# Kernel optimization log

Hardware: AMD Instinct MI355X
Metric: run time of the kernel (lower is better)

Reference implementation:

```python
import jax, jax.numpy as jnp
import numpy as np

DIM = 768
HID = 1536
EPS = 1e-12
SCALE = float(np.sqrt(DIM))


def _layernorm(x, gamma, beta):
    mu = jnp.mean(x, axis=-1, keepdims=True)
    var = jnp.mean(jnp.square(x - mu), axis=-1, keepdims=True)
    return (x - mu) * jax.lax.rsqrt(var + EPS) * gamma + beta


def setup_inputs() -> dict:
    key = jax.random.key(0)
    ks = jax.random.split(key, 16)
    s = 1.0 / np.sqrt(DIM)
    sh = 1.0 / np.sqrt(HID)
    x = jax.random.normal(ks[0], (8, 2048, DIM), dtype=jnp.float32)
    return {
        "x": x,
        "Wq": jax.random.uniform(ks[1], (DIM, DIM), jnp.float32, -s, s),
        "bq": jax.random.uniform(ks[2], (DIM,), jnp.float32, -s, s),
        "Wk": jax.random.uniform(ks[3], (DIM, DIM), jnp.float32, -s, s),
        "bk": jax.random.uniform(ks[4], (DIM,), jnp.float32, -s, s),
        "Wv": jax.random.uniform(ks[5], (DIM, DIM), jnp.float32, -s, s),
        "bv": jax.random.uniform(ks[6], (DIM,), jnp.float32, -s, s),
        "Wp": jax.random.uniform(ks[7], (DIM, DIM), jnp.float32, -s, s),
        "bp": jax.random.uniform(ks[8], (DIM,), jnp.float32, -s, s),
        "g1": jnp.ones((DIM,), jnp.float32),
        "be1": jnp.zeros((DIM,), jnp.float32),
        "W1": jax.random.uniform(ks[9], (HID, DIM), jnp.float32, -s, s),
        "b1": jax.random.uniform(ks[10], (HID,), jnp.float32, -s, s),
        "W2": jax.random.uniform(ks[11], (DIM, HID), jnp.float32, -sh, sh),
        "b2": jax.random.uniform(ks[12], (DIM,), jnp.float32, -sh, sh),
        "g2": jnp.ones((DIM,), jnp.float32),
        "be2": jnp.zeros((DIM,), jnp.float32),
    }


def reference(x, Wq, bq, Wk, bk, Wv, bv, Wp, bp, g1, be1, W1, b1, W2, b2, g2, be2):
    # NOTE: original code does NOT split into heads; single full-dim bmm attention.
    Q = jnp.einsum("bsd,ed->bse", x, Wq) + bq  # [B,S,D]
    K = jnp.einsum("bsd,ed->bse", x, Wk) + bk
    V = jnp.einsum("bsd,ed->bse", x, Wv) + bv
    alpha = jnp.einsum("bqd,bkd->bqk", Q, K) / SCALE  # [B,S,S]
    alpha = jax.nn.softmax(alpha, axis=-1)
    attn = jnp.einsum("bqk,bkd->bqd", alpha, V)
    attn = jnp.einsum("bsd,ed->bse", attn, Wp) + bp  # linear_proj
    h = _layernorm(x + attn, g1, be1)
    mlp = jax.nn.gelu(jnp.einsum("bsd,hd->bsh", h, W1) + b1, approximate=False)
    mlp = jnp.einsum("bsh,dh->bsd", mlp, W2) + b2
    return _layernorm(h + mlp, g2, be2)
```

## Files before the change

kernel.cpp:

```cpp
#include <hip/hip_runtime.h>
#include <math.h>

#define D_MODEL 768
#define D_HID   1536
#define N_BATCH 8
#define SEQLEN  2048
#define NROWS   (N_BATCH*SEQLEN)

typedef unsigned short u16;
typedef unsigned char  u8;
typedef __attribute__((ext_vector_type(8))) short bfrag;
typedef __attribute__((ext_vector_type(4))) float facc;

__device__ __forceinline__ u16 f2bf(float f) {
  unsigned u = __float_as_uint(f);
  u += 0x7fffu + ((u >> 16) & 1u);
  return (u16)(u >> 16);
}
__device__ __forceinline__ float bf2f(u16 u) {
  return __uint_as_float((unsigned)u << 16);
}
__device__ __forceinline__ u8 f2fp8(float f) {
  return (u8)(__builtin_amdgcn_cvt_pk_fp8_f32(f, f, 0, 0) & 0xff);
}

__device__ __forceinline__ void async16(const void* g, void* l) {
  __builtin_amdgcn_global_load_lds((const __attribute__((address_space(1))) void*)g,
                                   (__attribute__((address_space(3))) void*)l,
                                   16, 0, 0);
}
__device__ __forceinline__ void wg_barrier() {
  asm volatile("" ::: "memory");
  __builtin_amdgcn_s_barrier();
  asm volatile("" ::: "memory");
}
#define VMCNT(n) asm volatile("s_waitcnt vmcnt(" #n ")" ::: "memory")

__global__ __launch_bounds__(256) void cvt_all(
    const float* __restrict__ x,  const float* __restrict__ Wq,
    const float* __restrict__ Wk, const float* __restrict__ Wv,
    const float* __restrict__ Wp, const float* __restrict__ W1,
    const float* __restrict__ W2, const float* __restrict__ bq,
    const float* __restrict__ bk, const float* __restrict__ bv,
    u16* __restrict__ XB, u16* __restrict__ WQKV, u16* __restrict__ WPB,
    u16* __restrict__ W1B, u16* __restrict__ W2B, float* __restrict__ BQKV,
    float* __restrict__ LSUM) {
  long i = (long)blockIdx.x * 256 + threadIdx.x;
  const float* src; u16* dst; long off;
  if      (i < 3145728) { src = x;  dst = XB;             off = i; }
  else if (i < 3293184) { src = Wq; dst = WQKV;           off = i - 3145728; }
  else if (i < 3440640) { src = Wk; dst = WQKV + 589824;  off = i - 3293184; }
  else if (i < 3588096) { src = Wv; dst = WQKV + 1179648; off = i - 3440640; }
  else if (i < 3735552) { src = Wp; dst = WPB;            off = i - 3588096; }
  else if (i < 4030464) { src = W1; dst = W1B;            off = i - 3735552; }
  else if (i < 4325376) { src = W2; dst = W2B;            off = i - 4030464; }
  else if (i < 4325952) {
    long j = i - 4325376;
    const float* s = (j < 192) ? bq : (j < 384) ? bk : bv;
    long o = (j < 192) ? j : (j < 384) ? j - 192 : j - 384;
    ((float4*)BQKV)[j] = ((const float4*)s)[o];
    return;
  } else if (i < 4330048) {
    float4 zz = {0.f, 0.f, 0.f, 0.f};
    ((float4*)LSUM)[i - 4325952] = zz;
    return;
  } else return;
  float4 v = ((const float4*)src)[off];
  ushort4 o4;
  o4.x = f2bf(v.x); o4.y = f2bf(v.y); o4.z = f2bf(v.z); o4.w = f2bf(v.w);
  *reinterpret_cast<ushort4*>(dst + off * 4) = o4;
}

enum { EPI_EXP = 1, EPI_DIV = 2, EPI_GELU = 4, EPI_QKV = 5, EPI_RES = 6 };

template<int EPI>
__global__ __launch_bounds__(512, 2)
void gemm8(const u16* __restrict__ Aall, const u16* __restrict__ Ball,
           void* __restrict__ Cout,
           int M, int N, int K,
           long sA, long sB, long sC,
           const float* __restrict__ bias,
           const u16* __restrict__ resid,
           float* __restrict__ lsum,
           float scale)
{
  __shared__ __align__(16) char smem[131072];
  const int z = blockIdx.z;
  const u16* A = Aall + (long)z * sA;
  const u16* B = Ball + (long)z * sB;
  const int bm = blockIdx.x, bn = blockIdx.y;
  const int tid = (int)threadIdx.x;
  const int lane = tid & 63, wv = tid >> 6;
  const int wr = wv >> 2, wc = wv & 3;

  facc acc[8][4] = {};

  const int srow = tid >> 3;
  const int scol = (((tid & 7) ^ (srow & 7)) << 3);
  const u16* Abase = A + (long)(bm * 256) * K;
  const u16* Bbase = B + (long)(bn * 256) * K;
  const int fr = lane & 15, g0 = lane >> 4;
  const int nt = K >> 6;

  auto STAGE = [&](int t, int b) {
    u16* Asb = (u16*)(smem + b * 65536);
    u16* Bsb = (u16*)(smem + b * 65536 + 32768);
    const long k0 = (long)t * 64;
#pragma unroll
    for (int p = 0; p < 4; ++p)
      async16(Abase + (long)(p * 64 + srow) * K + k0 + scol, Asb + p * 4096 + wv * 512);
#pragma unroll
    for (int p = 0; p < 4; ++p)
      async16(Bbase + (long)(p * 64 + srow) * K + k0 + scol, Bsb + p * 4096 + wv * 512);
  };

#define G8_LDA(mh)                                                              \
  _Pragma("unroll") for (int i = 0; i < 4; ++i)                                 \
  _Pragma("unroll") for (int h = 0; h < 2; ++h) {                               \
    const int r = wr * 128 + (mh) * 64 + i * 16 + fr;                           \
    af[i][h] = *(const bfrag*)(As + r * 64 + (((g0 + h * 4) ^ (r & 7)) << 3));  \
  }
#define G8_LDB(nh)                                                              \
  _Pragma("unroll") for (int j = 0; j < 2; ++j)                                 \
  _Pragma("unroll") for (int h = 0; h < 2; ++h) {                               \
    const int r = wc * 64 + (nh) * 32 + j * 16 + fr;                            \
    bfv[j][h] = *(const bfrag*)(Bs + r * 64 + (((g0 + h * 4) ^ (r & 7)) << 3)); \
  }
#define G8_FMA(mh, nh)                                                          \
  __builtin_amdgcn_s_setprio(1);                                                \
  _Pragma("unroll") for (int i = 0; i < 4; ++i)                                 \
  _Pragma("unroll") for (int j = 0; j < 2; ++j)                                 \
  _Pragma("unroll") for (int h = 0; h < 2; ++h)                                 \
    acc[(mh) * 4 + i][(nh) * 2 + j] = __builtin_amdgcn_mfma_f32_16x16x32_bf16(  \
        af[i][h], bfv[j][h], acc[(mh) * 4 + i][(nh) * 2 + j], 0, 0, 0);         \
  __builtin_amdgcn_s_setprio(0);

  STAGE(0, 0);
  for (int t = 0; t < nt; ++t) {
    const int ct = t & 1;
    const u16* As = (const u16*)(smem + ct * 65536);
    const u16* Bs = (const u16*)(smem + ct * 65536 + 32768);
    if (t + 1 < nt) { STAGE(t + 1, ct ^ 1); VMCNT(8); }
    else            { VMCNT(0); }
    wg_barrier();
    bfrag af[4][2], bfv[2][2];
    G8_LDA(0) G8_LDB(0) G8_FMA(0, 0) wg_barrier();
    G8_LDB(1)           G8_FMA(0, 1) wg_barrier();
    G8_LDA(1)           G8_FMA(1, 1) wg_barrier();
    G8_LDB(0)           G8_FMA(1, 0) wg_barrier();
  }
#undef G8_LDA
#undef G8_LDB
#undef G8_FMA

  const int rb = bm * 256 + wr * 128;
  const int cb = bn * 256 + wc * 64;
  const int quad = lane >> 4;

  if constexpr (EPI == EPI_QKV) {
    const int c64 = bn * 4 + wc;
    const int which = c64 / 12;
    float bj[4];
#pragma unroll
    for (int j = 0; j < 4; ++j) bj[j] = bias[cb + j * 16 + fr];
    if (which == 2) {
      u8* VT_ = (u8*)resid;
      const int zb = rb >> 11;
      const int sbase = rb & 2047;
      const int dimb = (c64 - 24) * 64;
#pragma unroll
      for (int i = 0; i < 8; ++i)
#pragma unroll
        for (int j = 0; j < 4; ++j) {
          const int dim = dimb + j * 16 + fr;
          unsigned v01 = __builtin_amdgcn_cvt_pk_fp8_f32(acc[i][j][0] + bj[j],
                                                         acc[i][j][1] + bj[j], 0, 0);
          unsigned v23 = __builtin_amdgcn_cvt_pk_fp8_f32(acc[i][j][2] + bj[j],
                                                         acc[i][j][3] + bj[j], 0, 0);
          unsigned w = (v01 & 0xffffu) | (v23 << 16);
          *reinterpret_cast<unsigned*>(VT_ + (long)zb * D_MODEL * SEQLEN +
                                       (long)dim * SEQLEN + sbase + i * 16 + quad * 4) = w;
        }
      return;
    }
    u8* ep8 = (u8*)(smem + wv * 8192);
    u8* Cg = (u8*)Cout + (long)which * NROWS * D_MODEL;
    const int cbo = (c64 - which * 12) * 64;
#pragma unroll
    for (int i = 0; i < 8; ++i)
#pragma unroll
      for (int r = 0; r < 4; ++r) {
        const int lrow = i * 16 + quad * 4 + r;
#pragma unroll
        for (int j = 0; j < 4; ++j)
          ep8[lrow * 64 + j * 16 + fr] = f2fp8(acc[i][j][r] + bj[j]);
      }
#pragma unroll
    for (int it = 0; it < 8; ++it) {
      const int lr = it * 16 + (lane >> 2);
      const int ch = (lane & 3) << 4;
      int4 d = *(const int4*)(ep8 + lr * 64 + ch);
      *reinterpret_cast<int4*>(Cg + (long)(rb + lr) * D_MODEL + cbo + ch) = d;
    }
  } else if constexpr (EPI == EPI_GELU) {
    u16* ep16 = (u16*)(smem + wv * 16384);
    u16* Cg = (u16*)Cout + (long)z * sC;
    float bj[4];
#pragma unroll
    for (int j = 0; j < 4; ++j) bj[j] = bias[cb + j * 16 + fr];
#pragma unroll
    for (int i = 0; i < 8; ++i)
#pragma unroll
      for (int r = 0; r < 4; ++r) {
        const int lrow = i * 16 + quad * 4 + r;
#pragma unroll
        for (int j = 0; j < 4; ++j) {
          float tt = acc[i][j][r] + bj[j];
          float y = 0.7978845608f * (tt + 0.044715f * tt * tt * tt);
          float e = __expf(-2.f * fabsf(y));
          float th = (1.f - e) / (1.f + e);
          th = (y < 0.f) ? -th : th;
          ep16[lrow * 64 + j * 16 + fr] = f2bf(0.5f * tt * (1.f + th));
        }
      }
#pragma unroll
    for (int it = 0; it < 16; ++it) {
      const int lr = it * 8 + (lane >> 3);
      const int ch = (lane & 7) << 3;
      int4 d = *(const int4*)(ep16 + lr * 64 + ch);
      *reinterpret_cast<int4*>(Cg + (long)(rb + lr) * N + cb + ch) = d;
    }
  } else {
    float* ep32 = (float*)(smem + wv * 16384);
    u16* Cg = (u16*)Cout;
#pragma unroll
    for (int h2 = 0; h2 < 2; ++h2) {
#pragma unroll
      for (int i2 = 0; i2 < 4; ++i2) {
        const int i = h2 * 4 + i2;
#pragma unroll
        for (int r = 0; r < 4; ++r) {
          const int lrow = i2 * 16 + quad * 4 + r;
#pragma unroll
          for (int j = 0; j < 4; ++j)
            ep32[lrow * 64 + j * 16 + fr] = acc[i][j][r];
        }
      }
#pragma unroll
      for (int it = 0; it < 16; ++it) {
        const int lr = it * 4 + (lane >> 4);
        const int ch = (lane & 15) << 2;
        float4 d = *(const float4*)(ep32 + lr * 64 + ch);
        const int row = rb + h2 * 64 + lr;
        const int gcol = cb + ch;
        const long gi = (long)row * N + gcol;
        ushort4 rv = *(const ushort4*)(resid + gi);
        float4 bb = *(const float4*)(bias + gcol);
        ushort4 o;
        o.x = f2bf(d.x + bb.x + bf2f(rv.x));
        o.y = f2bf(d.y + bb.y + bf2f(rv.y));
        o.z = f2bf(d.z + bb.z + bf2f(rv.z));
        o.w = f2bf(d.w + bb.w + bf2f(rv.w));
        *reinterpret_cast<ushort4*>(Cg + gi) = o;
      }
    }
  }
  (void)lsum; (void)scale; (void)M;
}

template<int EPI>
__global__ __launch_bounds__(512, 2)
void gemm8_f8(const u8* __restrict__ Aall, const u8* __restrict__ Ball,
              void* __restrict__ Cout,
              int M, int N, int K,
              long sA, long sB, long sC,
              float* __restrict__ lsum, float scale)
{
  __shared__ __align__(16) char smem[131072];
  const int z = blockIdx.z;
  const u8* A = Aall + (long)z * sA;
  const u8* B = Ball + (long)z * sB;
  const int bm = blockIdx.x, bn = blockIdx.y;
  const int tid = (int)threadIdx.x;
  const int lane = tid & 63, wv = tid >> 6;
  const int wr = wv >> 2, wc = wv & 3;

  facc acc[8][4] = {};

  const int srow = tid >> 3;
  const int scolb = (((tid & 7) ^ (srow & 7)) << 4);
  const u8* Abase = A + (long)(bm * 256) * K;
  const u8* Bbase = B + (long)(bn * 256) * K;
  const int fr = lane & 15, g0 = lane >> 4;
  const int nt = K >> 7;

  auto STAGE = [&](int t, int b) {
    u8* Asb = (u8*)(smem + b * 65536);
    u8* Bsb = (u8*)(smem + b * 65536 + 32768);
    const long k0 = (long)t << 7;
#pragma unroll
    for (int p = 0; p < 4; ++p)
      async16(Abase + (long)(p * 64 + srow) * K + k0 + scolb, Asb + p * 8192 + wv * 1024);
#pragma unroll
    for (int p = 0; p < 4; ++p)
      async16(Bbase + (long)(p * 64 + srow) * K + k0 + scolb, Bsb + p * 8192 + wv * 1024);
  };

#define F8_LDA(mh)                                                                   \
  _Pragma("unroll") for (int i = 0; i < 4; ++i)                                      \
  _Pragma("unroll") for (int s = 0; s < 4; ++s) {                                    \
    const int r = wr * 128 + (mh) * 64 + i * 16 + fr;                                \
    const int c = s * 2 + (g0 >> 1);                                                 \
    af[i][s] = *(const long*)(As + r * 128 + ((c ^ (r & 7)) << 4) + ((g0 & 1) << 3)); \
  }
#define F8_LDB(nh)                                                                   \
  _Pragma("unroll") for (int j = 0; j < 2; ++j)                                      \
  _Pragma("unroll") for (int s = 0; s < 4; ++s) {                                    \
    const int r = wc * 64 + (nh) * 32 + j * 16 + fr;                                 \
    const int c = s * 2 + (g0 >> 1);                                                 \
    bfv[j][s] = *(const long*)(Bs + r * 128 + ((c ^ (r & 7)) << 4) + ((g0 & 1) << 3)); \
  }
#define F8_FMA(mh, nh)                                                               \
  __builtin_amdgcn_s_setprio(1);                                                     \
  _Pragma("unroll") for (int i = 0; i < 4; ++i)                                      \
  _Pragma("unroll") for (int j = 0; j < 2; ++j)                                      \
  _Pragma("unroll") for (int s = 0; s < 4; ++s)                                      \
    acc[(mh) * 4 + i][(nh) * 2 + j] = __builtin_amdgcn_mfma_f32_16x16x32_fp8_fp8(    \
        af[i][s], bfv[j][s], acc[(mh) * 4 + i][(nh) * 2 + j], 0, 0, 0);              \
  __builtin_amdgcn_s_setprio(0);

  STAGE(0, 0);
  for (int t = 0; t < nt; ++t) {
    const int ct = t & 1;
    const u8* As = (const u8*)(smem + ct * 65536);
    const u8* Bs = (const u8*)(smem + ct * 65536 + 32768);
    if (t + 1 < nt) { STAGE(t + 1, ct ^ 1); VMCNT(8); }
    else            { VMCNT(0); }
    wg_barrier();
    long af[4][4], bfv[2][4];
    F8_LDA(0) F8_LDB(0) F8_FMA(0, 0) wg_barrier();
    F8_LDB(1)           F8_FMA(0, 1) wg_barrier();
    F8_LDA(1)           F8_FMA(1, 1) wg_barrier();
    F8_LDB(0)           F8_FMA(1, 0) wg_barrier();
  }
#undef F8_LDA
#undef F8_LDB
#undef F8_FMA

  const int rb = bm * 256 + wr * 128;
  const int cb = bn * 256 + wc * 64;
  const int quad = lane >> 4;

  if constexpr (EPI == EPI_EXP) {
    u8* ep8 = (u8*)(smem + wv * 8192);
    u8* Cg = (u8*)Cout + (long)z * sC;
#pragma unroll
    for (int i = 0; i < 8; ++i) {
#pragma unroll
      for (int r = 0; r < 4; ++r) {
        const int lrow = i * 16 + quad * 4 + r;
        const int row = rb + lrow;
        float rs = 0.f;
#pragma unroll
        for (int j = 0; j < 4; ++j) {
          float e = __expf(acc[i][j][r] * scale - 3.0f);
          rs += e;
          ep8[lrow * 64 + j * 16 + fr] = f2fp8(e);
        }
        rs += __shfl_xor(rs, 1);
        rs += __shfl_xor(rs, 2);
        rs += __shfl_xor(rs, 4);
        rs += __shfl_xor(rs, 8);
        if (fr == 0) atomicAdd(&lsum[(long)z * M + row], rs);
      }
    }
#pragma unroll
    for (int it = 0; it < 8; ++it) {
      const int lr = it * 16 + (lane >> 2);
      const int ch = (lane & 3) << 4;
      int4 d = *(const int4*)(ep8 + lr * 64 + ch);
      *reinterpret_cast<int4*>(Cg + (long)(rb + lr) * N + cb + ch) = d;
    }
  } else {
    u16* ep16 = (u16*)(smem + wv * 16384);
    u16* Cg = (u16*)Cout + (long)z * sC;
#pragma unroll
    for (int i = 0; i < 8; ++i) {
#pragma unroll
      for (int r = 0; r < 4; ++r) {
        const int lrow = i * 16 + quad * 4 + r;
        const int row = rb + lrow;
        const float inv = 1.f / lsum[(long)z * M + row];
#pragma unroll
        for (int j = 0; j < 4; ++j)
          ep16[lrow * 64 + j * 16 + fr] = f2bf(acc[i][j][r] * inv);
      }
    }
#pragma unroll
    for (int it = 0; it < 16; ++it) {
      const int lr = it * 8 + (lane >> 3);
      const int ch = (lane & 7) << 3;
      int4 d = *(const int4*)(ep16 + lr * 64 + ch);
      *reinterpret_cast<int4*>(Cg + (long)(rb + lr) * N + cb + ch) = d;
    }
  }
}

__global__ __launch_bounds__(192) void layernorm_rows(const u16* __restrict__ in,
                                                      const float* __restrict__ gamma,
                                                      const float* __restrict__ beta,
                                                      float* __restrict__ outf,
                                                      u16* __restrict__ outb) {
  const int row = blockIdx.x;
  const int t = threadIdx.x;
  ushort4 uv = ((const ushort4*)(in + (long)row * D_MODEL))[t];
  float v0 = bf2f(uv.x), v1 = bf2f(uv.y), v2 = bf2f(uv.z), v3 = bf2f(uv.w);
  float s1 = v0 + v1 + v2 + v3;
  float s2 = v0 * v0 + v1 * v1 + v2 * v2 + v3 * v3;
#pragma unroll
  for (int o = 32; o; o >>= 1) { s1 += __shfl_xor(s1, o); s2 += __shfl_xor(s2, o); }
  __shared__ float r1[3], r2[3];
  const int wv = t >> 6, ln = t & 63;
  if (ln == 0) { r1[wv] = s1; r2[wv] = s2; }
  __syncthreads();
  s1 = r1[0] + r1[1] + r1[2];
  s2 = r2[0] + r2[1] + r2[2];
  const float mu = s1 * (1.f / 768.f);
  const float var = s2 * (1.f / 768.f) - mu * mu;
  const float rstd = rsqrtf(var + 1e-12f);
  float4 gv = ((const float4*)gamma)[t];
  float4 bv = ((const float4*)beta)[t];
  float o0 = (v0 - mu) * rstd * gv.x + bv.x;
  float o1 = (v1 - mu) * rstd * gv.y + bv.y;
  float o2 = (v2 - mu) * rstd * gv.z + bv.z;
  float o3 = (v3 - mu) * rstd * gv.w + bv.w;
  if (outf) {
    float4 ov = {o0, o1, o2, o3};
    ((float4*)(outf + (long)row * D_MODEL))[t] = ov;
  }
  if (outb) {
    ushort4 ob;
    ob.x = f2bf(o0); ob.y = f2bf(o1); ob.z = f2bf(o2); ob.w = f2bf(o3);
    ((ushort4*)(outb + (long)row * D_MODEL))[t] = ob;
  }
}

static const size_t OFF_WP   = 0;
static const size_t OFF_W1   = 1179648;
static const size_t OFF_W2   = 3538944;
static const size_t OFF_LSUM = 5898240;
static const size_t OFF_BQKV = 5963776;
static const size_t OFF_QB   = 6291456;
static const size_t OFF_KB   = 18874368;
static const size_t OFF_VT   = 31457280;
static const size_t OFF_EB   = 44040192;
static const size_t OFF_CTX  = 77594624;
static const size_t OFF_XB   = 102760448;
static const size_t OFF_WQKV = 127926272;
static const size_t OFF_M1B  = 131465216;

extern "C" void kernel_launch(void* const* d_in, const int* in_sizes, int n_in,
                              void* d_out, int out_size, void* d_ws, size_t ws_size,
                              hipStream_t stream) {
  const float* x   = (const float*)d_in[0];
  const float* Wq  = (const float*)d_in[1];
  const float* bq  = (const float*)d_in[2];
  const float* Wk  = (const float*)d_in[3];
  const float* bk  = (const float*)d_in[4];
  const float* Wv  = (const float*)d_in[5];
  const float* bv  = (const float*)d_in[6];
  const float* Wp  = (const float*)d_in[7];
  const float* bp  = (const float*)d_in[8];
  const float* g1  = (const float*)d_in[9];
  const float* be1 = (const float*)d_in[10];
  const float* W1  = (const float*)d_in[11];
  const float* b1  = (const float*)d_in[12];
  const float* W2  = (const float*)d_in[13];
  const float* b2  = (const float*)d_in[14];
  const float* g2  = (const float*)d_in[15];
  const float* be2 = (const float*)d_in[16];

  char* ws = (char*)d_ws;
  u16*   WPB  = (u16*)(ws + OFF_WP);
  u16*   W1B  = (u16*)(ws + OFF_W1);
  u16*   W2B  = (u16*)(ws + OFF_W2);
  float* LSUM = (float*)(ws + OFF_LSUM);
  float* BQKV = (float*)(ws + OFF_BQKV);
  u8*    QB   = (u8*)(ws + OFF_QB);
  u8*    KB   = (u8*)(ws + OFF_KB);
  u8*    VT   = (u8*)(ws + OFF_VT);
  u8*    EB   = (u8*)(ws + OFF_EB);
  u16*   CTX  = (u16*)(ws + OFF_CTX);
  u16*   XB   = (u16*)(ws + OFF_XB);
  u16*   WQKV = (u16*)(ws + OFF_WQKV);
  u16*   M1B  = (u16*)(ws + OFF_M1B);
  u16*   PB   = (u16*)(ws + OFF_QB);
  u16*   HB   = (u16*)(ws + OFF_EB);
  u16*   M2B  = (u16*)(ws + OFF_CTX);

  dim3 blk(256), b512(512), blkl(192);

  cvt_all<<<dim3(16915), blk, 0, stream>>>(x, Wq, Wk, Wv, Wp, W1, W2, bq, bk, bv,
                                           XB, WQKV, WPB, W1B, W2B, BQKV, LSUM);

  gemm8<EPI_QKV><<<dim3(64, 9, 1), b512, 0, stream>>>(XB, WQKV, QB,
      NROWS, 3 * D_MODEL, D_MODEL, 0, 0, 0, BQKV, (const u16*)VT, nullptr, 0.f);

  const float sc = 1.0f / sqrtf((float)D_MODEL);
  gemm8_f8<EPI_EXP><<<dim3(8, 8, 8), b512, 0, stream>>>(QB, KB, EB,
      SEQLEN, SEQLEN, D_MODEL,
      (long)SEQLEN * D_MODEL, (long)SEQLEN * D_MODEL, (long)SEQLEN * SEQLEN,
      LSUM, sc);
  gemm8_f8<EPI_DIV><<<dim3(8, 3, 8), b512, 0, stream>>>(EB, VT, CTX,
      SEQLEN, D_MODEL, SEQLEN,
      (long)SEQLEN * SEQLEN, (long)D_MODEL * SEQLEN, (long)SEQLEN * D_MODEL,
      LSUM, 0.f);
  gemm8<EPI_RES><<<dim3(64, 3, 1), b512, 0, stream>>>(CTX, WPB, PB,
      NROWS, D_MODEL, D_MODEL, 0, 0, 0, bp, XB, nullptr, 0.f);
  layernorm_rows<<<dim3(NROWS), blkl, 0, stream>>>(PB, g1, be1, nullptr, HB);
  gemm8<EPI_GELU><<<dim3(64, 6, 1), b512, 0, stream>>>(HB, W1B, M1B,
      NROWS, D_HID, D_MODEL, 0, 0, 0, b1, nullptr, nullptr, 0.f);
  gemm8<EPI_RES><<<dim3(64, 3, 1), b512, 0, stream>>>(M1B, W2B, M2B,
      NROWS, D_MODEL, D_HID, 0, 0, 0, b2, HB, nullptr, 0.f);
  layernorm_rows<<<dim3(NROWS), blkl, 0, stream>>>(M2B, g2, be2, (float*)d_out, nullptr);

  (void)in_sizes; (void)n_in; (void)out_size; (void)ws_size;
}
```

Before: 527.3 us.

## Interleave global-to-LDS prefetch with MFMA phases in 8-wave GEMM main loops

Replaces the per-tile STAGE-then-compute loop in both the bf16 and fp8 GEMM kernels with an unrolled two-tile ping-pong schedule. Each of the four MFMA sub-phases now issues a quarter of the next tiles' async global-to-LDS loads, and explicit lgkmcnt waits plus sched barriers bracket the MFMA blocks. The goal is to spread memory traffic across the compute phases and keep the matrix units busy while loads are in flight. It adds extra barriers per phase and relies on carefully tuned vmcnt counts and a reorganized B-tile load mapping, which risks correctness if K/128 or K/64 is odd or the counts are off.

After: 525.8 us. About the same (-0.3%).

```diff
diff --git a/kernel.cpp b/kernel.cpp
--- a/kernel.cpp
+++ b/kernel.cpp
@@ -35,6 +35,8 @@
   asm volatile("" ::: "memory");
 }
 #define VMCNT(n) asm volatile("s_waitcnt vmcnt(" #n ")" ::: "memory")
+#define LGK0 do { asm volatile("s_waitcnt lgkmcnt(0)" ::: "memory"); \
+                  __builtin_amdgcn_sched_barrier(0); } while (0)
 
 __global__ __launch_bounds__(256) void cvt_all(
     const float* __restrict__ x,  const float* __restrict__ Wq,
@@ -100,18 +102,27 @@
   const u16* Abase = A + (long)(bm * 256) * K;
   const u16* Bbase = B + (long)(bn * 256) * K;
   const int fr = lane & 15, g0 = lane >> 4;
-  const int nt = K >> 6;
-
-  auto STAGE = [&](int t, int b) {
-    u16* Asb = (u16*)(smem + b * 65536);
-    u16* Bsb = (u16*)(smem + b * 65536 + 32768);
+  const int nt = K >> 6, niter = nt >> 1;
+
+  auto SA = [&](int t, int b, int m) {
+    char* Asb = smem + b * 65536;
     const long k0 = (long)t * 64;
 #pragma unroll
-    for (int p = 0; p < 4; ++p)
-      async16(Abase + (long)(p * 64 + srow) * K + k0 + scol, Asb + p * 4096 + wv * 512);
-#pragma unroll
-    for (int p = 0; p < 4; ++p)
-      async16(Bbase + (long)(p * 64 + srow) * K + k0 + scol, Bsb + p * 4096 + wv * 512);
+    for (int l = 0; l < 2; ++l) {
+      const int p = m + l * 2;
+      async16(Abase + (long)(p * 64 + srow) * K + k0 + scol,
+              Asb + p * 8192 + wv * 1024);
+    }
+  };
+  auto SB = [&](int t, int b, int u) {
+    char* Bsb = smem + b * 65536 + 32768;
+    const long k0 = (long)t * 64;
+#pragma unroll
+    for (int l = 0; l < 2; ++l) {
+      const int rbase = (l * 2 + (wv >> 2)) * 64 + u * 32 + (wv & 3) * 8;
+      async16(Bbase + (long)(rbase + (lane >> 3)) * K + k0 + scol,
+              Bsb + rbase * 128);
+    }
   };
 
 #define G8_LDA(mh)                                                              \
@@ -126,32 +137,51 @@
     const int r = wc * 64 + (nh) * 32 + j * 16 + fr;                            \
     bfv[j][h] = *(const bfrag*)(Bs + r * 64 + (((g0 + h * 4) ^ (r & 7)) << 3)); \
   }
-#define G8_FMA(mh, nh)                                                          \
+#define G8_TAIL(mh, nh)                                                         \
+  wg_barrier();                                                                 \
+  LGK0;                                                                         \
   __builtin_amdgcn_s_setprio(1);                                                \
   _Pragma("unroll") for (int i = 0; i < 4; ++i)                                 \
   _Pragma("unroll") for (int j = 0; j < 2; ++j)                                 \
   _Pragma("unroll") for (int h = 0; h < 2; ++h)                                 \
     acc[(mh) * 4 + i][(nh) * 2 + j] = __builtin_amdgcn_mfma_f32_16x16x32_bf16(  \
         af[i][h], bfv[j][h], acc[(mh) * 4 + i][(nh) * 2 + j], 0, 0, 0);         \
-  __builtin_amdgcn_s_setprio(0);
-
-  STAGE(0, 0);
-  for (int t = 0; t < nt; ++t) {
-    const int ct = t & 1;
-    const u16* As = (const u16*)(smem + ct * 65536);
-    const u16* Bs = (const u16*)(smem + ct * 65536 + 32768);
-    if (t + 1 < nt) { STAGE(t + 1, ct ^ 1); VMCNT(8); }
-    else            { VMCNT(0); }
-    wg_barrier();
-    bfrag af[4][2], bfv[2][2];
-    G8_LDA(0) G8_LDB(0) G8_FMA(0, 0) wg_barrier();
-    G8_LDB(1)           G8_FMA(0, 1) wg_barrier();
-    G8_LDA(1)           G8_FMA(1, 1) wg_barrier();
-    G8_LDB(0)           G8_FMA(1, 0) wg_barrier();
-  }
+  __builtin_amdgcn_s_setprio(0);                                                \
+  wg_barrier();
+
+  SA(0, 0, 0); SB(0, 0, 0); SA(0, 0, 1); SB(0, 0, 1);
+  SA(1, 1, 0); SB(1, 1, 1); SA(1, 1, 1);
+  VMCNT(6);
+  wg_barrier();
+
+  bfrag af[4][2], bfv[2][2];
+  for (int it2 = 0; it2 < niter; ++it2) {
+    const int e = it2 * 2;
+    const int t1 = e + 1;
+    const int t2 = (e + 2 < nt) ? e + 2 : nt - 1;
+    const int t3 = (e + 3 < nt) ? e + 3 : nt - 1;
+    {
+      const u16* As = (const u16*)smem;
+      const u16* Bs = (const u16*)(smem + 32768);
+      G8_LDA(0) G8_LDB(0) SB(t1, 1, 0);           G8_TAIL(0, 0)
+      G8_LDB(1)           SA(t2, 0, 0);           G8_TAIL(0, 1)
+      G8_LDA(1)           SB(t2, 0, 1);           G8_TAIL(1, 1)
+      G8_LDB(0)           SA(t2, 0, 1); VMCNT(6); G8_TAIL(1, 0)
+    }
+    {
+      const u16* As = (const u16*)(smem + 65536);
+      const u16* Bs = (const u16*)(smem + 65536 + 32768);
+      G8_LDA(0) G8_LDB(0) SB(t2, 0, 0);           G8_TAIL(0, 0)
+      G8_LDB(1)           SA(t3, 1, 0);           G8_TAIL(0, 1)
+      G8_LDA(1)           SB(t3, 1, 1);           G8_TAIL(1, 1)
+      G8_LDB(0)           SA(t3, 1, 1); VMCNT(6); G8_TAIL(1, 0)
+    }
+  }
+  VMCNT(0);
+  wg_barrier();
 #undef G8_LDA
 #undef G8_LDB
-#undef G8_FMA
+#undef G8_TAIL
 
   const int rb = bm * 256 + wr * 128;
   const int cb = bn * 256 + wc * 64;
@@ -292,60 +322,88 @@
   const u8* Abase = A + (long)(bm * 256) * K;
   const u8* Bbase = B + (long)(bn * 256) * K;
   const int fr = lane & 15, g0 = lane >> 4;
-  const int nt = K >> 7;
-
-  auto STAGE = [&](int t, int b) {
-    u8* Asb = (u8*)(smem + b * 65536);
-    u8* Bsb = (u8*)(smem + b * 65536 + 32768);
+  const int nt = K >> 7, niter = nt >> 1;
+
+  auto SA = [&](int t, int b, int m) {
+    char* Asb = smem + b * 65536;
     const long k0 = (long)t << 7;
 #pragma unroll
-    for (int p = 0; p < 4; ++p)
-      async16(Abase + (long)(p * 64 + srow) * K + k0 + scolb, Asb + p * 8192 + wv * 1024);
-#pragma unroll
-    for (int p = 0; p < 4; ++p)
-      async16(Bbase + (long)(p * 64 + srow) * K + k0 + scolb, Bsb + p * 8192 + wv * 1024);
+    for (int l = 0; l < 2; ++l) {
+      const int p = m + l * 2;
+      async16(Abase + (long)(p * 64 + srow) * K + k0 + scolb,
+              Asb + p * 8192 + wv * 1024);
+    }
   };
-
-#define F8_LDA(mh)                                                                   \
-  _Pragma("unroll") for (int i = 0; i < 4; ++i)                                      \
-  _Pragma("unroll") for (int s = 0; s < 4; ++s) {                                    \
-    const int r = wr * 128 + (mh) * 64 + i * 16 + fr;                                \
-    const int c = s * 2 + (g0 >> 1);                                                 \
+  auto SB = [&](int t, int b, int u) {
+    char* Bsb = smem + b * 65536 + 32768;
+    const long k0 = (long)t << 7;
+#pragma unroll
+    for (int l = 0; l < 2; ++l) {
+      const int rbase = (l * 2 + (wv >> 2)) * 64 + u * 32 + (wv & 3) * 8;
+      async16(Bbase + (long)(rbase + (lane >> 3)) * K + k0 + scolb,
+              Bsb + rbase * 128);
+    }
+  };
+
+#define F8_LDA(mh)                                                                    \
+  _Pragma("unroll") for (int i = 0; i < 4; ++i)                                       \
+  _Pragma("unroll") for (int s = 0; s < 4; ++s) {                                     \
+    const int r = wr * 128 + (mh) * 64 + i * 16 + fr;                                 \
+    const int c = s * 2 + (g0 >> 1);                                                  \
     af[i][s] = *(const long*)(As + r * 128 + ((c ^ (r & 7)) << 4) + ((g0 & 1) << 3)); \
   }
-#define F8_LDB(nh)                                                                   \
-  _Pragma("unroll") for (int j = 0; j < 2; ++j)                                      \
-  _Pragma("unroll") for (int s = 0; s < 4; ++s) {                                    \
-    const int r = wc * 64 + (nh) * 32 + j * 16 + fr;                                 \
-    const int c = s * 2 + (g0 >> 1);                                                 \
+#define F8_LDB(nh)                                                                    \
+  _Pragma("unroll") for (int j = 0; j < 2; ++j)                                       \
+  _Pragma("unroll") for (int s = 0; s < 4; ++s) {                                     \
+    const int r = wc * 64 + (nh) * 32 + j * 16 + fr;                                  \
+    const int c = s * 2 + (g0 >> 1);                                                  \
     bfv[j][s] = *(const long*)(Bs + r * 128 + ((c ^ (r & 7)) << 4) + ((g0 & 1) << 3)); \
   }
-#define F8_FMA(mh, nh)                                                               \
-  __builtin_amdgcn_s_setprio(1);                                                     \
-  _Pragma("unroll") for (int i = 0; i < 4; ++i)                                      \
-  _Pragma("unroll") for (int j = 0; j < 2; ++j)                                      \
-  _Pragma("unroll") for (int s = 0; s < 4; ++s)                                      \
-    acc[(mh) * 4 + i][(nh) * 2 + j] = __builtin_amdgcn_mfma_f32_16x16x32_fp8_fp8(    \
-        af[i][s], bfv[j][s], acc[(mh) * 4 + i][(nh) * 2 + j], 0, 0, 0);              \
-  __builtin_amdgcn_s_setprio(0);
-
-  STAGE(0, 0);
-  for (int t = 0; t < nt; ++t) {
-    const int ct = t & 1;
-    const u8* As = (const u8*)(smem + ct * 65536);
-    const u8* Bs = (const u8*)(smem + ct * 65536 + 32768);
-    if (t + 1 < nt) { STAGE(t + 1, ct ^ 1); VMCNT(8); }
-    else            { VMCNT(0); }
-    wg_barrier();
-    long af[4][4], bfv[2][4];
-    F8_LDA(0) F8_LDB(0) F8_FMA(0, 0) wg_barrier();
-    F8_LDB(1)           F8_FMA(0, 1) wg_barrier();
-    F8_LDA(1)           F8_FMA(1, 1) wg_barrier();
-    F8_LDB(0)           F8_FMA(1, 0) wg_barrier();
-  }
+#define F8_TAIL(mh, nh)                                                               \
+  wg_barrier();                                                                       \
+  LGK0;                                                                               \
+  __builtin_amdgcn_s_setprio(1);                                                      \
+  _Pragma("unroll") for (int i = 0; i < 4; ++i)                                       \
+  _Pragma("unroll") for (int j = 0; j < 2; ++j)                                       \
+  _Pragma("unroll") for (int s = 0; s < 4; ++s)                                       \
+    acc[(mh) * 4 + i][(nh) * 2 + j] = __builtin_amdgcn_mfma_f32_16x16x32_fp8_fp8(     \
+        af[i][s], bfv[j][s], acc[(mh) * 4 + i][(nh) * 2 + j], 0, 0, 0);               \
+  __builtin_amdgcn_s_setprio(0);                                                      \
+  wg_barrier();
+
+  SA(0, 0, 0); SB(0, 0, 0); SA(0, 0, 1); SB(0, 0, 1);
+  SA(1, 1, 0); SB(1, 1, 1); SA(1, 1, 1);
+  VMCNT(6);
+  wg_barrier();
+
+  long af[4][4], bfv[2][4];
+  for (int it2 = 0; it2 < niter; ++it2) {
+    const int e = it2 * 2;
+    const int t1 = e + 1;
+    const int t2 = (e + 2 < nt) ? e + 2 : nt - 1;
+    const int t3 = (e + 3 < nt) ? e + 3 : nt - 1;
+    {
+      const u8* As = (const u8*)smem;
+      const u8* Bs = (const u8*)(smem + 32768);
+      F8_LDA(0) F8_LDB(0) SB(t1, 1, 0);           F8_TAIL(0, 0)
+      F8_LDB(1)           SA(t2, 0, 0);           F8_TAIL(0, 1)
+      F8_LDA(1)           SB(t2, 0, 1);           F8_TAIL(1, 1)
+      F8_LDB(0)           SA(t2, 0, 1); VMCNT(6); F8_TAIL(1, 0)
+    }
+    {
+      const u8* As = (const u8*)(smem + 65536);
+      const u8* Bs = (const u8*)(smem + 65536 + 32768);
+      F8_LDA(0) F8_LDB(0) SB(t2, 0, 0);           F8_TAIL(0, 0)
+      F8_LDB(1)           SA(t3, 1, 0);           F8_TAIL(0, 1)
+      F8_LDA(1)           SB(t3, 1, 1);           F8_TAIL(1, 1)
+      F8_LDB(0)           SA(t3, 1, 1); VMCNT(6); F8_TAIL(1, 0)
+    }
+  }
+  VMCNT(0);
+  wg_barrier();
 #undef F8_LDA
 #undef F8_LDB
-#undef F8_FMA
+#undef F8_TAIL
 
   const int rb = bm * 256 + wr * 128;
   const int cb = bn * 256 + wc * 64;
```
